# Performance work log

Measured on AMD Instinct MI355X. Metric: run time of the kernel, lower is better.

## Reference

```python
import jax, jax.numpy as jnp
import numpy as np


def setup_inputs() -> dict:
    key = jax.random.key(0)
    k1, k2, k3, k4 = jax.random.split(key, 4)
    B, C, N, T = 16, 64, 2048, 24
    x = jax.random.normal(k1, (B, C, N, T), dtype=jnp.float32)
    adj = jax.random.uniform(k2, (N, N), dtype=jnp.float32)
    # Learned parameters (initialized to zeros in the original; random here
    # so the reference exercises nontrivial math).
    Gw = jax.random.normal(k3, (T, T), dtype=jnp.float32) * 0.1
    alpha = jax.random.normal(k4, (C,), dtype=jnp.float32) * 0.1
    return {"x": x, "adj": adj, "Gw": Gw, "alpha": alpha}


def reference(x, adj, Gw, alpha):
    # k = q = einsum('bcnt,c->bnt')  (channel-reduced features)
    k = jnp.einsum('bcnt,c->bnt', x, alpha)
    # scores[b,n,m] = k[b,n,:] @ Gw @ k[b,m,:]
    kG = jnp.einsum('bnt,ts->bns', k, Gw)          # [B,N,T]
    scores = jnp.einsum('bns,bms->bnm', kG, k)     # [B,N,N]
    att = jax.nn.softmax(scores, axis=-1)
    # adjacency-masked weighted aggregation over neighbors
    return jnp.einsum('bnm,bcmt->bcnt', att * adj, x)
```

## Files before the change

kernel.cpp:

```cpp
#include <hip/hip_runtime.h>
#include <hip/hip_bf16.h>

#define BB 16
#define CC 64
#define NN 2048
#define TT 24
#define JJ (CC*TT)
#define NT (NN*TT)

typedef unsigned short u16;
typedef unsigned int u32;
typedef __bf16 bf16x8 __attribute__((ext_vector_type(8)));
typedef u16 u16x8 __attribute__((ext_vector_type(8)));
typedef float f32x4 __attribute__((ext_vector_type(4)));
typedef u32 u32x4 __attribute__((ext_vector_type(4)));

static __device__ __forceinline__ u16 f2bf(float f) {
  union { float f; u32 u; } v; v.f = f;
  u32 u = v.u;
  u += 0x7fffu + ((u >> 16) & 1u);
  return (u16)(u >> 16);
}
static __device__ __forceinline__ float bf2f(u16 h) {
  union { u32 u; float f; } v; v.u = ((u32)h) << 16; return v.f;
}
static __device__ __forceinline__ bf16x8 ld_bf8(const u16* p) {
  return __builtin_bit_cast(bf16x8, *(const u16x8*)p);
}
#define MFMA16(a,b,c) __builtin_amdgcn_mfma_f32_16x16x32_bf16((a),(b),(c),0,0,0)

static __device__ __forceinline__ void gload16(const u16* g, u16* lds) {
  __builtin_amdgcn_global_load_lds(
      (const __attribute__((address_space(1))) u32*)g,
      (__attribute__((address_space(3))) u32*)lds, 16, 0, 0);
}

__global__ __launch_bounds__(256) void kA(
    const float* __restrict__ x, const float* __restrict__ alpha,
    u16* __restrict__ xT, float* __restrict__ kpart) {
  int bid = blockIdx.x;
  int b  = bid >> 5;
  int mt = (bid >> 1) & 15;
  int ch = bid & 1;
  int m0 = mt * 128;
  int tid = threadIdx.x;
  __shared__ float tile[128][25];
  float kacc[12];
  #pragma unroll
  for (int e = 0; e < 12; ++e) kacc[e] = 0.f;

  for (int c = ch*32; c < ch*32 + 32; ++c) {
    const float4* src4 = (const float4*)(x + ((size_t)(b*CC + c)*NN + m0)*TT);
    float a = alpha[c];
    float4 v[3];
    #pragma unroll
    for (int q = 0; q < 3; ++q) v[q] = src4[tid*3 + q];
    __syncthreads();
    #pragma unroll
    for (int q = 0; q < 3; ++q) {
      int idx = tid*3 + q;
      int mm = idx / 6, off = (idx - mm*6)*4;
      tile[mm][off]   = v[q].x; tile[mm][off+1] = v[q].y;
      tile[mm][off+2] = v[q].z; tile[mm][off+3] = v[q].w;
      kacc[q*4+0] += a*v[q].x; kacc[q*4+1] += a*v[q].y;
      kacc[q*4+2] += a*v[q].z; kacc[q*4+3] += a*v[q].w;
    }
    __syncthreads();
    #pragma unroll
    for (int qq = 0; qq < 6; ++qq) {
      int idx = tid*6 + qq;
      int t = idx >> 6, mp = idx & 63;
      u32 lo = f2bf(tile[2*mp][t]);
      u32 hi = f2bf(tile[2*mp+1][t]);
      ((u32*)(xT + ((size_t)((b*CC + c)*TT + t))*NN + m0))[mp] = lo | (hi << 16);
    }
  }
  float* kp = kpart + (size_t)ch*BB*NT + (size_t)b*NT + (size_t)m0*TT + tid*12;
  #pragma unroll
  for (int q = 0; q < 3; ++q)
    *(float4*)(kp + q*4) = make_float4(kacc[q*4], kacc[q*4+1], kacc[q*4+2], kacc[q*4+3]);
}

__global__ __launch_bounds__(256) void k2_prep(
    const float* __restrict__ kpart, const float* __restrict__ Gw,
    u16* __restrict__ kGhi, u16* __restrict__ kGlo,
    u16* __restrict__ kPhi, u16* __restrict__ kPlo) {
  __shared__ float gw[TT*TT];
  for (int i = threadIdx.x; i < TT*TT; i += 256) gw[i] = Gw[i];
  __syncthreads();
  int row = blockIdx.x * blockDim.x + threadIdx.x;
  if (row >= BB*NN) return;
  float kr[TT];
  const float4* s0 = (const float4*)(kpart + (size_t)row*TT);
  const float4* s1 = (const float4*)(kpart + (size_t)BB*NT + (size_t)row*TT);
  #pragma unroll
  for (int q = 0; q < 6; ++q) {
    float4 a = s0[q], bv = s1[q];
    kr[4*q]   = a.x + bv.x; kr[4*q+1] = a.y + bv.y;
    kr[4*q+2] = a.z + bv.z; kr[4*q+3] = a.w + bv.w;
  }
  float o[TT];
  #pragma unroll
  for (int s = 0; s < TT; ++s) o[s] = 0.f;
  #pragma unroll
  for (int t = 0; t < TT; ++t) {
    float kv = kr[t];
    #pragma unroll
    for (int s = 0; s < TT; ++s) o[s] += kv * gw[t*TT + s];
  }
  size_t rb = (size_t)row * 32;
  u32* ghi = (u32*)(kGhi + rb); u32* glo = (u32*)(kGlo + rb);
  u32* phi = (u32*)(kPhi + rb); u32* plo = (u32*)(kPlo + rb);
  #pragma unroll
  for (int sp = 0; sp < 16; ++sp) {
    float v0 = (2*sp   < TT) ? o[2*sp]   : 0.f;
    float v1 = (2*sp+1 < TT) ? o[2*sp+1] : 0.f;
    u16 h0 = f2bf(v0), h1 = f2bf(v1);
    u16 l0 = f2bf(v0 - bf2f(h0)), l1 = f2bf(v1 - bf2f(h1));
    ghi[sp] = (u32)h0 | ((u32)h1 << 16);
    glo[sp] = (u32)l0 | ((u32)l1 << 16);
    float w0 = (2*sp   < TT) ? kr[2*sp]   : 0.f;
    float w1 = (2*sp+1 < TT) ? kr[2*sp+1] : 0.f;
    u16 ph0 = f2bf(w0), ph1 = f2bf(w1);
    u16 pl0 = f2bf(w0 - bf2f(ph0)), pl1 = f2bf(w1 - bf2f(ph1));
    phi[sp] = (u32)ph0 | ((u32)ph1 << 16);
    plo[sp] = (u32)pl0 | ((u32)pl1 << 16);
  }
}

__global__ __launch_bounds__(256) void kW(
    const u16* __restrict__ kGhi, const u16* __restrict__ kGlo,
    const u16* __restrict__ kPhi, const u16* __restrict__ kPlo,
    const float* __restrict__ adj, u16* __restrict__ Wm,
    float* __restrict__ Zpart) {
  int bid = blockIdx.x;
  int b = bid >> 8, nt = (bid >> 4) & 15, mt = bid & 15;
  int tid = threadIdx.x;
  int w = tid >> 6, l = tid & 63;
  __shared__ u16 wlds[128][128];
  size_t kgb = ((size_t)b*NN + nt*128) * 32;
  bf16x8 ahi[2], alo[2];
  #pragma unroll
  for (int nf = 0; nf < 2; ++nf) {
    size_t off = kgb + (size_t)(w*32 + nf*16 + (l & 15))*32 + (l >> 4)*8;
    ahi[nf] = ld_bf8(kGhi + off);
    alo[nf] = ld_bf8(kGlo + off);
  }
  f32x4 acc[2][8];
  #pragma unroll
  for (int mf = 0; mf < 8; ++mf) {
    size_t off = ((size_t)b*NN + mt*128 + mf*16 + (l & 15))*32 + (l >> 4)*8;
    bf16x8 bhi = ld_bf8(kPhi + off);
    bf16x8 blo = ld_bf8(kPlo + off);
    #pragma unroll
    for (int nf = 0; nf < 2; ++nf) {
      f32x4 a = {0.f, 0.f, 0.f, 0.f};
      a = MFMA16(ahi[nf], blo, a);
      a = MFMA16(alo[nf], bhi, a);
      a = MFMA16(ahi[nf], bhi, a);
      acc[nf][mf] = a;
    }
  }
  #pragma unroll
  for (int nf = 0; nf < 2; ++nf)
    #pragma unroll
    for (int r = 0; r < 4; ++r) {
      int nl = w*32 + nf*16 + (l >> 4)*4 + r;
      float rs = 0.f;
      #pragma unroll
      for (int mf = 0; mf < 8; ++mf) {
        int ml = mf*16 + (l & 15);
        float e = __expf(acc[nf][mf][r]);
        rs += e;
        float wv = e * adj[(size_t)(nt*128 + nl)*NN + mt*128 + ml];
        wlds[nl][ml] = f2bf(wv);
      }
      #pragma unroll
      for (int st = 1; st < 16; st <<= 1) rs += __shfl_xor(rs, st);
      if ((l & 15) == 0)
        Zpart[((size_t)b*NN + nt*128 + nl)*16 + mt] = rs;
    }
  __syncthreads();
  int row = tid >> 1, half = tid & 1;
  const u32x4* s4 = (const u32x4*)&wlds[row][half*64];
  u32x4* d4 = (u32x4*)(Wm + ((size_t)(b*NN + nt*128 + row))*NN + mt*128 + half*64);
  #pragma unroll
  for (int q = 0; q < 8; ++q) d4[q] = s4[q];
}

__global__ __launch_bounds__(512, 2) void k4_gemm(
    const u16* __restrict__ Wm, const u16* __restrict__ xT,
    const float* __restrict__ Zpart, float* __restrict__ out) {
  __shared__ __align__(16) u16 sA[2*256*64];
  __shared__ __align__(16) u16 sB[2*256*64];
  __shared__ float rinv[256];

  int bid = blockIdx.x;
  int wg = (bid & 7) * 96 + (bid >> 3);
  int b = wg / 48; int rem = wg - b*48;
  int nt = rem / 6, jt = rem - nt*6;

  int tid = threadIdx.x;
  int w = tid >> 6, l = tid & 63;
  int wr = w >> 2, wc = w & 3;
  int l15 = l & 15, l4 = l >> 4, lx = l & 7;

  int g0 = ((l4)     ^ lx) << 3;
  int g1 = ((4 + l4) ^ lx) << 3;
  int rbA = wr*8192 + l15*64;
  int rbB = wc*4096 + l15*64;

  int srow = tid >> 3, sslot = tid & 7;
  int sgx = (sslot ^ (srow & 7)) << 3;
  const size_t ROW64 = (size_t)64 * NN;
  const u16* pA = Wm + (size_t)b*NN*NN + (size_t)(nt*256 + srow)*NN + sgx;
  const u16* pB = xT + (size_t)b*JJ*NN + (size_t)(jt*256 + srow)*NN + sgx;
  int wbase = w << 9;

  f32x4 acc[8][4];
  #pragma unroll
  for (int f = 0; f < 8; ++f)
    #pragma unroll
    for (int cf = 0; cf < 4; ++cf) acc[f][cf] = (f32x4){0.f,0.f,0.f,0.f};

  if (tid < 256) {
    const float4* zp = (const float4*)(Zpart + ((size_t)b*NN + nt*256 + tid)*16);
    float4 a = zp[0], bz = zp[1], c = zp[2], d = zp[3];
    float s = a.x+a.y+a.z+a.w + bz.x+bz.y+bz.z+bz.w
            + c.x+c.y+c.z+c.w + d.x+d.y+d.z+d.w;
    rinv[tid] = 1.f / s;
  }
  #pragma unroll
  for (int i = 0; i < 4; ++i) gload16(pA + (size_t)i*ROW64, sA + i*4096 + wbase);
  #pragma unroll
  for (int i = 0; i < 4; ++i) gload16(pB + (size_t)i*ROW64, sB + i*4096 + wbase);
  pA += 64; pB += 64;
  asm volatile("s_waitcnt vmcnt(0)" ::: "memory");
  __builtin_amdgcn_sched_barrier(0);
  __builtin_amdgcn_s_barrier();
  __builtin_amdgcn_sched_barrier(0);

  for (int kt = 0; kt < 32; ++kt) {
    int pb = (kt & 1) << 14;
    int qb = pb ^ 16384;
    if (kt < 31) {
      #pragma unroll
      for (int i = 0; i < 4; ++i) gload16(pA + (size_t)i*ROW64, sA + qb + i*4096 + wbase);
      #pragma unroll
      for (int i = 0; i < 4; ++i) gload16(pB + (size_t)i*ROW64, sB + qb + i*4096 + wbase);
      pA += 64; pB += 64;
    }
    __builtin_amdgcn_sched_barrier(0);

    bf16x8 a0[8], b0[4], a1[8], b1[4];
    #pragma unroll
    for (int cf = 0; cf < 4; ++cf) b0[cf] = ld_bf8(sB + pb + rbB + cf*1024 + g0);
    #pragma unroll
    for (int f = 0; f < 8; ++f) a0[f] = ld_bf8(sA + pb + rbA + f*1024 + g0);
    __builtin_amdgcn_sched_barrier(0);
    #pragma unroll
    for (int cf = 0; cf < 4; ++cf) b1[cf] = ld_bf8(sB + pb + rbB + cf*1024 + g1);
    #pragma unroll
    for (int f = 0; f < 8; ++f) a1[f] = ld_bf8(sA + pb + rbA + f*1024 + g1);

    asm volatile("s_waitcnt lgkmcnt(15)" ::: "memory");
    __builtin_amdgcn_sched_barrier(0);
    __builtin_amdgcn_s_setprio(1);
    #pragma unroll
    for (int f = 0; f < 4; ++f)
      #pragma unroll
      for (int cf = 0; cf < 4; ++cf)
        acc[f][cf] = MFMA16(a0[f], b0[cf], acc[f][cf]);
    __builtin_amdgcn_s_setprio(0);
    asm volatile("s_waitcnt lgkmcnt(12)" ::: "memory");
    __builtin_amdgcn_sched_barrier(0);
    __builtin_amdgcn_s_setprio(1);
    #pragma unroll
    for (int f = 4; f < 8; ++f)
      #pragma unroll
      for (int cf = 0; cf < 4; ++cf)
        acc[f][cf] = MFMA16(a0[f], b0[cf], acc[f][cf]);
    __builtin_amdgcn_s_setprio(0);
    asm volatile("s_waitcnt lgkmcnt(4)" ::: "memory");
    __builtin_amdgcn_sched_barrier(0);
    __builtin_amdgcn_s_setprio(1);
    #pragma unroll
    for (int f = 0; f < 4; ++f)
      #pragma unroll
      for (int cf = 0; cf < 4; ++cf)
        acc[f][cf] = MFMA16(a1[f], b1[cf], acc[f][cf]);
    __builtin_amdgcn_s_setprio(0);
    asm volatile("s_waitcnt lgkmcnt(0)" ::: "memory");
    __builtin_amdgcn_sched_barrier(0);
    __builtin_amdgcn_s_setprio(1);
    #pragma unroll
    for (int f = 4; f < 8; ++f)
      #pragma unroll
      for (int cf = 0; cf < 4; ++cf)
        acc[f][cf] = MFMA16(a1[f], b1[cf], acc[f][cf]);
    __builtin_amdgcn_s_setprio(0);

    asm volatile("s_waitcnt vmcnt(0)" ::: "memory");
    __builtin_amdgcn_sched_barrier(0);
    __builtin_amdgcn_s_barrier();
    __builtin_amdgcn_sched_barrier(0);
  }

  int cj[4], tj4[4];
  #pragma unroll
  for (int cf = 0; cf < 4; ++cf) {
    int j = jt*256 + wc*64 + cf*16 + l15;
    cj[cf] = j / TT; tj4[cf] = j - cj[cf]*TT;
  }
  #pragma unroll
  for (int f = 0; f < 8; ++f)
    #pragma unroll
    for (int r = 0; r < 4; ++r) {
      int nl = wr*128 + f*16 + l4*4 + r;
      float rv = rinv[nl];
      #pragma unroll
      for (int cf = 0; cf < 4; ++cf)
        out[((size_t)(b*CC + cj[cf])*NN + nt*256 + nl)*TT + tj4[cf]] = acc[f][cf][r] * rv;
    }
}

extern "C" void kernel_launch(void* const* d_in, const int* in_sizes, int n_in,
                              void* d_out, int out_size, void* d_ws, size_t ws_size,
                              hipStream_t stream) {
  const float* x     = (const float*)d_in[0];
  const float* adj   = (const float*)d_in[1];
  const float* Gw    = (const float*)d_in[2];
  const float* alpha = (const float*)d_in[3];
  float* out = (float*)d_out;

  const size_t XT_B = (size_t)BB*JJ*NN*2;
  const size_t W_B  = (size_t)BB*NN*NN*2;
  const size_t KS_B = (size_t)BB*NN*32*2;
  char* base = (char*)d_ws;
  u16*   xT    = (u16*)base;
  u16*   Wm    = (u16*)(base + XT_B);
  float* kpart = (float*)(base + XT_B);
  u16*   kGhi  = (u16*)(base + XT_B + W_B);
  u16*   kGlo  = (u16*)(base + XT_B + W_B + KS_B);
  u16*   kPhi  = (u16*)(base + XT_B + W_B + 2*KS_B);
  u16*   kPlo  = (u16*)(base + XT_B + W_B + 3*KS_B);
  float* Zpart = (float*)(base + XT_B + W_B + 4*KS_B);

  kA<<<512, 256, 0, stream>>>(x, alpha, xT, kpart);
  k2_prep<<<BB*NN/256, 256, 0, stream>>>(kpart, Gw, kGhi, kGlo, kPhi, kPlo);
  kW<<<BB*16*16, 256, 0, stream>>>(kGhi, kGlo, kPhi, kPlo, adj, Wm, Zpart);
  k4_gemm<<<768, 512, 0, stream>>>(Wm, xT, Zpart, out);
}
```

Before: 416.2 us.

## Shrink final GEMM tile to 256x128 with K=32 steps for higher occupancy

Retiles the aggregation GEMM from 256x256 output tiles with 64-wide K steps to 256x128 tiles with 32-wide K steps, doubling the grid to 1536 blocks. It also raises launch bounds to 4 blocks per CU, shrinks LDS, reworks the swizzle and cuts accumulators to 16 per thread. The aim is more waves and blocks in flight for better latency hiding and a fuller machine. The cost is more re-reading of the Wm operand, since each row tile is now loaded by twice as many blocks, plus twice as many barrier iterations with less MFMA work between them.

```diff
diff --git a/kernel.cpp b/kernel.cpp
--- a/kernel.cpp
+++ b/kernel.cpp
@@ -188,38 +188,37 @@
   for (int q = 0; q < 8; ++q) d4[q] = s4[q];
 }
 
-__global__ __launch_bounds__(512, 2) void k4_gemm(
+__global__ __launch_bounds__(512, 4) void k4_gemm(
     const u16* __restrict__ Wm, const u16* __restrict__ xT,
     const float* __restrict__ Zpart, float* __restrict__ out) {
-  __shared__ __align__(16) u16 sA[2*256*64];
-  __shared__ __align__(16) u16 sB[2*256*64];
+  __shared__ __align__(16) u16 sA[2*256*32];
+  __shared__ __align__(16) u16 sB[2*128*32];
   __shared__ float rinv[256];
 
   int bid = blockIdx.x;
-  int wg = (bid & 7) * 96 + (bid >> 3);
-  int b = wg / 48; int rem = wg - b*48;
-  int nt = rem / 6, jt = rem - nt*6;
+  int wg = (bid & 7) * 192 + (bid >> 3);
+  int b = wg / 96; int rem = wg - b*96;
+  int nt = rem / 12, jt = rem - nt*12;
 
   int tid = threadIdx.x;
   int w = tid >> 6, l = tid & 63;
-  int wr = w >> 2, wc = w & 3;
-  int l15 = l & 15, l4 = l >> 4, lx = l & 7;
-
-  int g0 = ((l4)     ^ lx) << 3;
-  int g1 = ((4 + l4) ^ lx) << 3;
-  int rbA = wr*8192 + l15*64;
-  int rbB = wc*4096 + l15*64;
-
-  int srow = tid >> 3, sslot = tid & 7;
-  int sgx = (sslot ^ (srow & 7)) << 3;
-  const size_t ROW64 = (size_t)64 * NN;
+  int wr = w >> 1, wc = w & 1;
+  int l15 = l & 15, l4 = l >> 4;
+
+  int g = (l4 ^ ((l15 >> 1) & 3)) << 3;
+  int rbA = wr*2048 + l15*32;
+  int rbB = wc*2048 + l15*32;
+
+  int srow = tid >> 2, sslot = tid & 3;
+  int sgx = (sslot ^ ((srow >> 1) & 3)) << 3;
+  const size_t ROW128 = (size_t)128 * NN;
   const u16* pA = Wm + (size_t)b*NN*NN + (size_t)(nt*256 + srow)*NN + sgx;
-  const u16* pB = xT + (size_t)b*JJ*NN + (size_t)(jt*256 + srow)*NN + sgx;
-  int wbase = w << 9;
-
-  f32x4 acc[8][4];
-  #pragma unroll
-  for (int f = 0; f < 8; ++f)
+  const u16* pB = xT + (size_t)b*JJ*NN + (size_t)(jt*128 + srow)*NN + sgx;
+  int wb = w << 9;
+
+  f32x4 acc[4][4];
+  #pragma unroll
+  for (int f = 0; f < 4; ++f)
     #pragma unroll
     for (int cf = 0; cf < 4; ++cf) acc[f][cf] = (f32x4){0.f,0.f,0.f,0.f};
 
@@ -230,74 +229,57 @@
             + c.x+c.y+c.z+c.w + d.x+d.y+d.z+d.w;
     rinv[tid] = 1.f / s;
   }
-  #pragma unroll
-  for (int i = 0; i < 4; ++i) gload16(pA + (size_t)i*ROW64, sA + i*4096 + wbase);
-  #pragma unroll
-  for (int i = 0; i < 4; ++i) gload16(pB + (size_t)i*ROW64, sB + i*4096 + wbase);
-  pA += 64; pB += 64;
+  gload16(pA,          sA + wb);
+  gload16(pA + ROW128, sA + 4096 + wb);
+  gload16(pB,          sB + wb);
+  pA += 32; pB += 32;
   asm volatile("s_waitcnt vmcnt(0)" ::: "memory");
   __builtin_amdgcn_sched_barrier(0);
   __builtin_amdgcn_s_barrier();
   __builtin_amdgcn_sched_barrier(0);
 
-  for (int kt = 0; kt < 32; ++kt) {
-    int pb = (kt & 1) << 14;
-    int qb = pb ^ 16384;
-    if (kt < 31) {
-      #pragma unroll
-      for (int i = 0; i < 4; ++i) gload16(pA + (size_t)i*ROW64, sA + qb + i*4096 + wbase);
-      #pragma unroll
-      for (int i = 0; i < 4; ++i) gload16(pB + (size_t)i*ROW64, sB + qb + i*4096 + wbase);
-      pA += 64; pB += 64;
-    }
-    __builtin_amdgcn_sched_barrier(0);
-
-    bf16x8 a0[8], b0[4], a1[8], b1[4];
-    #pragma unroll
-    for (int cf = 0; cf < 4; ++cf) b0[cf] = ld_bf8(sB + pb + rbB + cf*1024 + g0);
-    #pragma unroll
-    for (int f = 0; f < 8; ++f) a0[f] = ld_bf8(sA + pb + rbA + f*1024 + g0);
-    __builtin_amdgcn_sched_barrier(0);
-    #pragma unroll
-    for (int cf = 0; cf < 4; ++cf) b1[cf] = ld_bf8(sB + pb + rbB + cf*1024 + g1);
-    #pragma unroll
-    for (int f = 0; f < 8; ++f) a1[f] = ld_bf8(sA + pb + rbA + f*1024 + g1);
-
-    asm volatile("s_waitcnt lgkmcnt(15)" ::: "memory");
+  for (int kt = 0; kt < 64; ++kt) {
+    int pbA = (kt & 1) << 13;
+    int qbA = pbA ^ 8192;
+    int pbB = (kt & 1) << 12;
+    int qbB = pbB ^ 4096;
+    if (kt < 63) {
+      gload16(pA,          sA + qbA + wb);
+      gload16(pA + ROW128, sA + qbA + 4096 + wb);
+      gload16(pB,          sB + qbB + wb);
+      pA += 32; pB += 32;
+    }
+    __builtin_amdgcn_sched_barrier(0);
+
+    bf16x8 av[4], bv[4];
+    #pragma unroll
+    for (int cf = 0; cf < 4; ++cf) bv[cf] = ld_bf8(sB + pbB + rbB + cf*512 + g);
+    #pragma unroll
+    for (int f = 0; f < 4; ++f) av[f] = ld_bf8(sA + pbA + rbA + f*512 + g);
+
+    asm volatile("s_waitcnt lgkmcnt(3)" ::: "memory");
     __builtin_amdgcn_sched_barrier(0);
     __builtin_amdgcn_s_setprio(1);
     #pragma unroll
-    for (int f = 0; f < 4; ++f)
-      #pragma unroll
-      for (int cf = 0; cf < 4; ++cf)
-        acc[f][cf] = MFMA16(a0[f], b0[cf], acc[f][cf]);
+    for (int cf = 0; cf < 4; ++cf) acc[0][cf] = MFMA16(av[0], bv[cf], acc[0][cf]);
     __builtin_amdgcn_s_setprio(0);
-    asm volatile("s_waitcnt lgkmcnt(12)" ::: "memory");
+    asm volatile("s_waitcnt lgkmcnt(2)" ::: "memory");
     __builtin_amdgcn_sched_barrier(0);
     __builtin_amdgcn_s_setprio(1);
     #pragma unroll
-    for (int f = 4; f < 8; ++f)
-      #pragma unroll
-      for (int cf = 0; cf < 4; ++cf)
-        acc[f][cf] = MFMA16(a0[f], b0[cf], acc[f][cf]);
+    for (int cf = 0; cf < 4; ++cf) acc[1][cf] = MFMA16(av[1], bv[cf], acc[1][cf]);
     __builtin_amdgcn_s_setprio(0);
-    asm volatile("s_waitcnt lgkmcnt(4)" ::: "memory");
+    asm volatile("s_waitcnt lgkmcnt(1)" ::: "memory");
     __builtin_amdgcn_sched_barrier(0);
     __builtin_amdgcn_s_setprio(1);
     #pragma unroll
-    for (int f = 0; f < 4; ++f)
-      #pragma unroll
-      for (int cf = 0; cf < 4; ++cf)
-        acc[f][cf] = MFMA16(a1[f], b1[cf], acc[f][cf]);
+    for (int cf = 0; cf < 4; ++cf) acc[2][cf] = MFMA16(av[2], bv[cf], acc[2][cf]);
     __builtin_amdgcn_s_setprio(0);
     asm volatile("s_waitcnt lgkmcnt(0)" ::: "memory");
     __builtin_amdgcn_sched_barrier(0);
     __builtin_amdgcn_s_setprio(1);
     #pragma unroll
-    for (int f = 4; f < 8; ++f)
-      #pragma unroll
-      for (int cf = 0; cf < 4; ++cf)
-        acc[f][cf] = MFMA16(a1[f], b1[cf], acc[f][cf]);
+    for (int cf = 0; cf < 4; ++cf) acc[3][cf] = MFMA16(av[3], bv[cf], acc[3][cf]);
     __builtin_amdgcn_s_setprio(0);
 
     asm volatile("s_waitcnt vmcnt(0)" ::: "memory");
@@ -309,14 +291,14 @@
   int cj[4], tj4[4];
   #pragma unroll
   for (int cf = 0; cf < 4; ++cf) {
-    int j = jt*256 + wc*64 + cf*16 + l15;
+    int j = jt*128 + wc*64 + cf*16 + l15;
     cj[cf] = j / TT; tj4[cf] = j - cj[cf]*TT;
   }
   #pragma unroll
-  for (int f = 0; f < 8; ++f)
+  for (int f = 0; f < 4; ++f)
     #pragma unroll
     for (int r = 0; r < 4; ++r) {
-      int nl = wr*128 + f*16 + l4*4 + r;
+      int nl = wr*64 + f*16 + l4*4 + r;
       float rv = rinv[nl];
       #pragma unroll
       for (int cf = 0; cf < 4; ++cf)
@@ -349,5 +331,5 @@
   kA<<<512, 256, 0, stream>>>(x, alpha, xT, kpart);
   k2_prep<<<BB*NN/256, 256, 0, stream>>>(kpart, Gw, kGhi, kGlo, kPhi, kPlo);
   kW<<<BB*16*16, 256, 0, stream>>>(kGhi, kGlo, kPhi, kPlo, adj, Wm, Zpart);
-  k4_gemm<<<768, 512, 0, stream>>>(Wm, xT, Zpart, out);
-}
+  k4_gemm<<<1536, 512, 0, stream>>>(Wm, xT, Zpart, out);
+}
```

New measurement: 409.5 us. Within noise of the previous version (-1.6%).
